# Optimization experiments

Measured on AMD Instinct MI355X. Metric: run time of the kernel, lower is better.

The kernel has to match this reference:

```python
import jax, jax.numpy as jnp
import numpy as np

DIM = 768
NUM_HEADS = 12
HEAD_DIM = DIM // NUM_HEADS
SCALE = HEAD_DIM ** -0.5
B, N = 8, 1024


def setup_inputs() -> dict:
    key = jax.random.key(0)
    k1, k2, k3, k4, k5 = jax.random.split(key, 5)
    x = jax.random.normal(k1, (B, N, DIM), dtype=jnp.float32)
    # qkv: Linear(dim, 3*dim, bias=False); proj: Linear(dim, dim) with bias
    w_qkv = jax.random.normal(k2, (3 * DIM, DIM), dtype=jnp.float32) * (DIM ** -0.5)
    w_proj = jax.random.normal(k3, (DIM, DIM), dtype=jnp.float32) * (DIM ** -0.5)
    b_proj = jnp.zeros((DIM,), dtype=jnp.float32)
    # learned attention mask parameter, shape (H, L, L) with L >= N
    att_mask = jax.random.normal(k4, (NUM_HEADS, N, N), dtype=jnp.float32)
    return {"x": x, "w_qkv": w_qkv, "w_proj": w_proj, "b_proj": b_proj, "att_mask": att_mask}


def reference(x, w_qkv, w_proj, b_proj, att_mask):
    Bx, Nx, C = x.shape
    # qkv projection -> (3, B, H, N, head_dim)
    qkv = (x @ w_qkv.T).reshape(Bx, Nx, 3, NUM_HEADS, C // NUM_HEADS)
    qkv = jnp.transpose(qkv, (2, 0, 3, 1, 4))
    q, k, v = qkv[0], qkv[1], qkv[2]  # gpd_ratio==active_ratio==1 -> scaling factor 1
    # scores [B, H, N, N]
    attn = jnp.einsum('bhnd,bhmd->bhnm', q, k) * SCALE
    # custom sigmoid mask gating before softmax (broadcast over batch)
    attn = attn * jax.nn.sigmoid(att_mask[:, :Nx, :Nx])[None, :, :, :]
    attn = jax.nn.softmax(attn, axis=-1)
    out = jnp.einsum('bhnm,bhmd->bhnd', attn, v)
    out = jnp.transpose(out, (0, 2, 1, 3)).reshape(Bx, Nx, C)
    return out @ w_proj.T + b_proj
```

## Files before the change

kernel.cpp:

```cpp
#include <hip/hip_runtime.h>
#include <math.h>
#include <stdint.h>

typedef unsigned short u16;
typedef __attribute__((ext_vector_type(8))) short short8;
typedef __attribute__((ext_vector_type(4))) float f32x4;

#define GATE_SCALE 0.18033688011112042f

#if __has_builtin(__builtin_amdgcn_exp2f)
#define FEXP2(x) __builtin_amdgcn_exp2f(x)
#else
#define FEXP2(x) exp2f(x)
#endif

__device__ __forceinline__ u16 f2b(float f) {
    union { float f; unsigned u; } v; v.f = f;
    unsigned r = v.u + 0x7fffu + ((v.u >> 16) & 1u);
    return (u16)(r >> 16);
}
__device__ __forceinline__ u16 f2b_hu(float f) {
    union { float f; unsigned u; } v; v.f = f;
    return (u16)((v.u + 0x8000u) >> 16);
}
__device__ __forceinline__ float b2f(u16 u) {
    union { float f; unsigned u; } v; v.u = ((unsigned)u) << 16; return v.f;
}

#define GLL16(gsrc, ldsbase) __builtin_amdgcn_global_load_lds(                    \
    (__attribute__((address_space(1))) void*)(uintptr_t)(gsrc),                   \
    (__attribute__((address_space(3))) void*)(uint32_t)(uintptr_t)(ldsbase),      \
    16, 0, 0)

#define NX4  1572864
#define NW14 442368
#define NW24 147456
#define NXW4 (NX4 + NW14 + NW24)

__global__ __launch_bounds__(256) void prep_xw(
    const float4* __restrict__ x, const float4* __restrict__ wq,
    const float4* __restrict__ wp,
    ushort4* __restrict__ xb, ushort4* __restrict__ wqb,
    ushort4* __restrict__ wpb)
{
    size_t i = (size_t)blockIdx.x * 256 + threadIdx.x;
    float4 v; ushort4* dst; size_t j;
    if (i < NX4)            { j = i;               v = x[j];  dst = xb;  }
    else if (i < NX4 + NW14){ j = i - NX4;         v = wq[j]; dst = wqb; }
    else                    { j = i - (NX4 + NW14);v = wp[j]; dst = wpb; }
    ushort4 o; o.x = f2b(v.x); o.y = f2b(v.y); o.z = f2b(v.z); o.w = f2b(v.w);
    dst[j] = o;
}

__global__ __launch_bounds__(256) void prep_gate(
    const float4* __restrict__ mask4, u16* __restrict__ gp)
{
    __shared__ u16 L[64][72];
    const int bid = blockIdx.x;
    const int kt = bid & 15, qt = (bid >> 4) & 15, h = bid >> 8;
    const int t = threadIdx.x;

    #pragma unroll
    for (int s = 0; s < 4; ++s) {
        const int idx = t + s * 256;
        const int row = idx >> 4, c4 = idx & 15;
        float4 v = mask4[(size_t)(h * 1024 + qt * 64 + row) * 256 + kt * 16 + c4];
        L[row][c4 * 4 + 0] = f2b(GATE_SCALE / (1.f + __expf(-v.x)));
        L[row][c4 * 4 + 1] = f2b(GATE_SCALE / (1.f + __expf(-v.y)));
        L[row][c4 * 4 + 2] = f2b(GATE_SCALE / (1.f + __expf(-v.z)));
        L[row][c4 * 4 + 3] = f2b(GATE_SCALE / (1.f + __expf(-v.w)));
    }
    __syncthreads();

    const int w = t >> 6, l = t & 63;
    const int fq = l >> 4, fr = l & 15;
    union { u16 u[16]; float4 f[2]; } vals;
    #pragma unroll
    for (int i = 0; i < 4; ++i)
        #pragma unroll
        for (int nt = 0; nt < 4; ++nt)
            vals.u[i * 4 + nt] = L[16 * w + 4 * fq + i][nt * 16 + fr];
    float4* dst = (float4*)(gp + (size_t)bid * 4096 + (size_t)t * 16);
    dst[0] = vals.f[0];
    dst[1] = vals.f[1];
}

__global__ __launch_bounds__(256) void qkv_gemm(
    const u16* __restrict__ xb, const u16* __restrict__ wb,
    u16* __restrict__ qb, u16* __restrict__ kb, u16* __restrict__ vb)
{
    __shared__ u16 As[3][4096];
    __shared__ u16 Bs[3][4096];
    const int t = threadIdx.x, l = t & 63, w = t >> 6;
    const int wm = (w & 1) * 64, wn = (w >> 1) * 64;

    const int orig = blockIdx.x + 18 * blockIdx.y;
    const int nid = (orig & 7) * 144 + (orig >> 3);
    const int m0 = (nid / 18) * 128, c0 = (nid % 18) * 128;

    f32x4 acc[4][4];
    #pragma unroll
    for (int i = 0; i < 4; ++i)
        #pragma unroll
        for (int j = 0; j < 4; ++j) { f32x4 z = {0.f,0.f,0.f,0.f}; acc[i][j] = z; }

    const int srow = l >> 2, sseg = l & 3;
    const int gcol = ((sseg ^ ((srow >> 1) & 3)) << 3);
    const u16* a0 = xb + (size_t)(m0 + w * 16 + srow) * 768 + gcol;
    const u16* a1 = a0 + (size_t)64 * 768;
    const u16* b0p = wb + (size_t)(c0 + w * 16 + srow) * 768 + gcol;
    const u16* b1p = b0p + (size_t)64 * 768;
    const int wofs = w * 512;

    const int fr = l & 15, fq = l >> 4;
    const int fseg = (fq ^ ((fr >> 1) & 3)) << 3;

    auto stage = [&](int bi, int koff) {
        GLL16(a0 + koff, &As[bi][wofs]);
        GLL16(a1 + koff, &As[bi][2048 + wofs]);
        GLL16(b0p + koff, &Bs[bi][wofs]);
        GLL16(b1p + koff, &Bs[bi][2048 + wofs]);
    };

    stage(0, 0);
    stage(1, 32);

    int cur = 0;
    for (int kt = 0; kt < 24; ++kt) {
        if (kt < 23) asm volatile("s_waitcnt vmcnt(4)" ::: "memory");
        else         asm volatile("s_waitcnt vmcnt(0)" ::: "memory");
        __builtin_amdgcn_s_barrier();
        if (kt < 22) {
            const int nn = (cur == 0) ? 2 : cur - 1;
            stage(nn, (kt + 2) * 32);
        }
        const u16* A = As[cur];
        const u16* B = Bs[cur];
        short8 af[4], bf[4];
        #pragma unroll
        for (int mt = 0; mt < 4; ++mt)
            af[mt] = *(const short8*)&A[(wm + mt * 16 + fr) * 32 + fseg];
        #pragma unroll
        for (int nt = 0; nt < 4; ++nt)
            bf[nt] = *(const short8*)&B[(wn + nt * 16 + fr) * 32 + fseg];
        #pragma unroll
        for (int mt = 0; mt < 4; ++mt)
            #pragma unroll
            for (int nt = 0; nt < 4; ++nt)
                acc[mt][nt] = __builtin_amdgcn_mfma_f32_16x16x32_bf16(
                    af[mt], bf[nt], acc[mt][nt], 0, 0, 0);
        cur = (cur == 2) ? 0 : cur + 1;
    }

    const int b = m0 >> 10;
    const int n0 = m0 & 1023;
    #pragma unroll
    for (int nt = 0; nt < 4; ++nt) {
        const int c = c0 + wn + nt * 16 + fr;
        const int which = c / 768;
        const int rem = c - which * 768;
        const int h = rem >> 6, d = rem & 63;
        if (which < 2) {
            u16* dst = ((which == 0) ? qb : kb)
                       + ((size_t)(b * 12 + h) * 1024) * 64 + d;
            #pragma unroll
            for (int mt = 0; mt < 4; ++mt)
                #pragma unroll
                for (int r = 0; r < 4; ++r) {
                    const int n = n0 + wm + mt * 16 + fq * 4 + r;
                    dst[(size_t)n * 64] = f2b(acc[mt][nt][r]);
                }
        } else {
            u16* dst = vb + ((size_t)(b * 12 + h) * 64 + d) * 1024
                          + n0 + wm + fq * 4;
            #pragma unroll
            for (int mt = 0; mt < 4; ++mt) {
                ushort4 pk;
                pk.x = f2b(acc[mt][nt][0]); pk.y = f2b(acc[mt][nt][1]);
                pk.z = f2b(acc[mt][nt][2]); pk.w = f2b(acc[mt][nt][3]);
                *(ushort4*)(dst + mt * 16) = pk;
            }
        }
    }
}

__global__ __launch_bounds__(256, 3) void flash_attn(
    const u16* __restrict__ qb, const u16* __restrict__ kb,
    const u16* __restrict__ vt, const u16* __restrict__ gperm,
    u16* __restrict__ aob)
{
    __shared__ u16 Qs[8192], Ks[4096], Vts[4096], Ps[4096];
    const int t = threadIdx.x, l = t & 63, w = t >> 6;
    const int bid = blockIdx.x;
    const int qtb = bid & 7, bh = bid >> 3;
    const int h = bh % 12, b = bh / 12;
    const int q0 = qtb * 128;

    const u16* hq = qb + (size_t)bh * 65536;
    const u16* hk = kb + (size_t)bh * 65536;
    const u16* hv = vt + (size_t)bh * 65536;
    const u16* hgb = gperm + ((size_t)h * 256 + qtb * 32) * 4096 + (w * 64 + l) * 16;

    const int sr = l >> 3, ss = l & 7;
    const int sg = ((ss ^ (sr & 7)) << 3);
    const int j0 = w * 2, j1 = j0 + 1;

    #pragma unroll
    for (int jq = 0; jq < 4; ++jq) {
        const int j = w * 4 + jq;
        GLL16(hq + (size_t)(q0 + j * 8 + sr) * 64 + sg, Qs + j * 512);
    }
    GLL16(hk + (size_t)(j0 * 8 + sr) * 64 + sg, Ks + j0 * 512);
    GLL16(hk + (size_t)(j1 * 8 + sr) * 64 + sg, Ks + j1 * 512);
    GLL16(hv + (size_t)(j0 * 8 + sr) * 1024 + sg, Vts + j0 * 512);
    GLL16(hv + (size_t)(j1 * 8 + sr) * 1024 + sg, Vts + j1 * 512);
    __syncthreads();

    const int fq = l >> 4, fr = l & 15;
    const int sega = ((fq ^ (fr & 7)) << 3);
    const int segb = (((4 + fq) ^ (fr & 7)) << 3);

    short8 aq[2][2];
    #pragma unroll
    for (int qh = 0; qh < 2; ++qh) {
        const int row = 16 * w + fr;
        aq[qh][0] = *(const short8*)&Qs[qh * 4096 + row * 64 + sega];
        aq[qh][1] = *(const short8*)&Qs[qh * 4096 + row * 64 + segb];
    }

    short8 gn[4];
    gn[0] = *(const short8*)(hgb);
    gn[1] = *(const short8*)(hgb + 8);
    gn[2] = *(const short8*)(hgb + 65536);
    gn[3] = *(const short8*)(hgb + 65536 + 8);

    float l_part[2][4] = {{0.f,0.f,0.f,0.f},{0.f,0.f,0.f,0.f}};
    f32x4 o[2][4];
    #pragma unroll
    for (int qh = 0; qh < 2; ++qh)
        #pragma unroll
        for (int nt = 0; nt < 4; ++nt) { f32x4 z = {0.f,0.f,0.f,0.f}; o[qh][nt] = z; }

    for (int kt = 0; kt < 16; ++kt) {
        short8 g[4];
        #pragma unroll
        for (int s = 0; s < 4; ++s) g[s] = gn[s];
        if (kt < 15) {
            const size_t go = (size_t)(kt + 1) * 4096;
            gn[0] = *(const short8*)(hgb + go);
            gn[1] = *(const short8*)(hgb + go + 8);
            gn[2] = *(const short8*)(hgb + 65536 + go);
            gn[3] = *(const short8*)(hgb + 65536 + go + 8);
        }

        f32x4 sv[2][4];
        #pragma unroll
        for (int nt = 0; nt < 4; ++nt) {
            short8 kf0 = *(const short8*)&Ks[(nt * 16 + fr) * 64 + sega];
            short8 kf1 = *(const short8*)&Ks[(nt * 16 + fr) * 64 + segb];
            f32x4 z0 = {0.f,0.f,0.f,0.f};
            z0 = __builtin_amdgcn_mfma_f32_16x16x32_bf16(aq[0][0], kf0, z0, 0, 0, 0);
            z0 = __builtin_amdgcn_mfma_f32_16x16x32_bf16(aq[0][1], kf1, z0, 0, 0, 0);
            sv[0][nt] = z0;
            f32x4 z1 = {0.f,0.f,0.f,0.f};
            z1 = __builtin_amdgcn_mfma_f32_16x16x32_bf16(aq[1][0], kf0, z1, 0, 0, 0);
            z1 = __builtin_amdgcn_mfma_f32_16x16x32_bf16(aq[1][1], kf1, z1, 0, 0, 0);
            sv[1][nt] = z1;
        }

        short8 ap[2][2];
        #pragma unroll
        for (int qh = 0; qh < 2; ++qh) {
            #pragma unroll
            for (int i = 0; i < 4; ++i) {
                const int pr = 4 * fq + i;
                #pragma unroll
                for (int nt = 0; nt < 4; ++nt) {
                    const int idx = i * 4 + nt;
                    const float gv = b2f((u16)(idx < 8 ? g[2 * qh][idx]
                                                       : g[2 * qh + 1][idx - 8]));
                    const float p = FEXP2(sv[qh][nt][i] * gv);
                    l_part[qh][i] += p;
                    const int col = nt * 16 + fr;
                    Ps[w * 1024 + pr * 64 + (((col >> 3) ^ (pr & 7)) << 3) + (col & 7)]
                        = f2b_hu(p);
                }
            }
            ap[qh][0] = *(const short8*)&Ps[w * 1024 + fr * 64 + sega];
            ap[qh][1] = *(const short8*)&Ps[w * 1024 + fr * 64 + segb];
        }

        #pragma unroll
        for (int nt = 0; nt < 4; ++nt) {
            short8 vf0 = *(const short8*)&Vts[(nt * 16 + fr) * 64 + sega];
            short8 vf1 = *(const short8*)&Vts[(nt * 16 + fr) * 64 + segb];
            o[0][nt] = __builtin_amdgcn_mfma_f32_16x16x32_bf16(ap[0][0], vf0, o[0][nt], 0, 0, 0);
            o[0][nt] = __builtin_amdgcn_mfma_f32_16x16x32_bf16(ap[0][1], vf1, o[0][nt], 0, 0, 0);
            o[1][nt] = __builtin_amdgcn_mfma_f32_16x16x32_bf16(ap[1][0], vf0, o[1][nt], 0, 0, 0);
            o[1][nt] = __builtin_amdgcn_mfma_f32_16x16x32_bf16(ap[1][1], vf1, o[1][nt], 0, 0, 0);
        }

        if (kt < 15) {
            __syncthreads();
            const size_t ko = (size_t)(kt + 1) * 64;
            GLL16(hk + (ko + j0 * 8 + sr) * 64 + sg, Ks + j0 * 512);
            GLL16(hk + (ko + j1 * 8 + sr) * 64 + sg, Ks + j1 * 512);
            GLL16(hv + (size_t)(j0 * 8 + sr) * 1024 + ko + sg, Vts + j0 * 512);
            GLL16(hv + (size_t)(j1 * 8 + sr) * 1024 + ko + sg, Vts + j1 * 512);
            __syncthreads();
        }
    }

    #pragma unroll
    for (int qh = 0; qh < 2; ++qh) {
        #pragma unroll
        for (int i = 0; i < 4; ++i) {
            float s = l_part[qh][i];
            s += __shfl_xor(s, 1, 16);
            s += __shfl_xor(s, 2, 16);
            s += __shfl_xor(s, 4, 16);
            s += __shfl_xor(s, 8, 16);
            const float inv = 1.f / s;
            const int n = q0 + qh * 64 + 16 * w + 4 * fq + i;
            const size_t rowoff = ((size_t)b * 1024 + n) * 768 + h * 64;
            #pragma unroll
            for (int nt = 0; nt < 4; ++nt)
                aob[rowoff + nt * 16 + fr] = f2b(o[qh][nt][i] * inv);
        }
    }
}

__global__ __launch_bounds__(256) void proj_gemm(
    const u16* __restrict__ aob, const u16* __restrict__ wb,
    const float* __restrict__ bproj, float* __restrict__ out)
{
    __shared__ u16 As[3][4096];
    __shared__ u16 Bs[3][4096];
    const int t = threadIdx.x, l = t & 63, w = t >> 6;
    const int wm = (w & 1) * 64, wn = (w >> 1) * 64;

    const int orig = blockIdx.x + 6 * blockIdx.y;
    const int nid = (orig & 7) * 48 + (orig >> 3);
    const int m0 = (nid / 6) * 128, c0 = (nid % 6) * 128;

    f32x4 acc[4][4];
    #pragma unroll
    for (int i = 0; i < 4; ++i)
        #pragma unroll
        for (int j = 0; j < 4; ++j) { f32x4 z = {0.f,0.f,0.f,0.f}; acc[i][j] = z; }

    const int srow = l >> 2, sseg = l & 3;
    const int gcol = ((sseg ^ ((srow >> 1) & 3)) << 3);
    const u16* a0 = aob + (size_t)(m0 + w * 16 + srow) * 768 + gcol;
    const u16* a1 = a0 + (size_t)64 * 768;
    const u16* b0p = wb + (size_t)(c0 + w * 16 + srow) * 768 + gcol;
    const u16* b1p = b0p + (size_t)64 * 768;
    const int wofs = w * 512;

    const int fr = l & 15, fq = l >> 4;
    const int fseg = (fq ^ ((fr >> 1) & 3)) << 3;

    auto stage = [&](int bi, int koff) {
        GLL16(a0 + koff, &As[bi][wofs]);
        GLL16(a1 + koff, &As[bi][2048 + wofs]);
        GLL16(b0p + koff, &Bs[bi][wofs]);
        GLL16(b1p + koff, &Bs[bi][2048 + wofs]);
    };

    stage(0, 0);
    stage(1, 32);

    int cur = 0;
    for (int kt = 0; kt < 24; ++kt) {
        if (kt < 23) asm volatile("s_waitcnt vmcnt(4)" ::: "memory");
        else         asm volatile("s_waitcnt vmcnt(0)" ::: "memory");
        __builtin_amdgcn_s_barrier();
        if (kt < 22) {
            const int nn = (cur == 0) ? 2 : cur - 1;
            stage(nn, (kt + 2) * 32);
        }
        const u16* A = As[cur];
        const u16* B = Bs[cur];
        short8 af[4], bf[4];
        #pragma unroll
        for (int mt = 0; mt < 4; ++mt)
            af[mt] = *(const short8*)&A[(wm + mt * 16 + fr) * 32 + fseg];
        #pragma unroll
        for (int nt = 0; nt < 4; ++nt)
            bf[nt] = *(const short8*)&B[(wn + nt * 16 + fr) * 32 + fseg];
        #pragma unroll
        for (int mt = 0; mt < 4; ++mt)
            #pragma unroll
            for (int nt = 0; nt < 4; ++nt)
                acc[mt][nt] = __builtin_amdgcn_mfma_f32_16x16x32_bf16(
                    af[mt], bf[nt], acc[mt][nt], 0, 0, 0);
        cur = (cur == 2) ? 0 : cur + 1;
    }

    #pragma unroll
    for (int nt = 0; nt < 4; ++nt) {
        const int c = c0 + wn + nt * 16 + fr;
        const float bias = bproj[c];
        #pragma unroll
        for (int mt = 0; mt < 4; ++mt)
            #pragma unroll
            for (int r = 0; r < 4; ++r) {
                const int m = m0 + wm + mt * 16 + fq * 4 + r;
                out[(size_t)m * 768 + c] = acc[mt][nt][r] + bias;
            }
    }
}

extern "C" void kernel_launch(void* const* d_in, const int* in_sizes, int n_in,
                              void* d_out, int out_size, void* d_ws, size_t ws_size,
                              hipStream_t stream)
{
    const float* x     = (const float*)d_in[0];
    const float* wqkv  = (const float*)d_in[1];
    const float* wproj = (const float*)d_in[2];
    const float* bproj = (const float*)d_in[3];
    const float* mask  = (const float*)d_in[4];
    float* out = (float*)d_out;

    char* ws = (char*)d_ws;
    u16* gperm  = (u16*)(ws);
    u16* xb     = (u16*)(ws + 25165824);
    u16* wqkvb  = (u16*)(ws + 37748736);
    u16* wprojb = (u16*)(ws + 41287680);
    u16* qb     = (u16*)(ws + 42467328);
    u16* kb     = (u16*)(ws + 55050240);
    u16* vb     = (u16*)(ws + 67633152);
    u16* aob    = (u16*)(ws + 80216064);

    prep_xw<<<NXW4 / 256, 256, 0, stream>>>(
        (const float4*)x, (const float4*)wqkv, (const float4*)wproj,
        (ushort4*)xb, (ushort4*)wqkvb, (ushort4*)wprojb);

    prep_gate<<<3072, 256, 0, stream>>>((const float4*)mask, gperm);

    qkv_gemm<<<dim3(18, 64), 256, 0, stream>>>(xb, wqkvb, qb, kb, vb);

    flash_attn<<<768, 256, 0, stream>>>(qb, kb, vb, gperm, aob);

    proj_gemm<<<dim3(6, 64), 256, 0, stream>>>(aob, wprojb, bproj, out);
}
```

Baseline: 242.5 us.

## Enlarge QKV GEMM tiles and read attention K/V/Q directly from global

The QKV GEMM moves from 128x128 tiles with 4 waves and triple buffering to 256x256 tiles with 8 waves and double buffering, waiting for all loads to finish each k-step. Flash attention drops its shared-memory staging of Q, K and V and loads the MFMA fragments straight from global memory, which removes the barriers and LDS traffic. The larger GEMM tile increases reuse, but the grid shrinks to 288 blocks and loads no longer overlap compute. The direct global reads in attention rely on L1/L2 for reuse across waves and can add memory latency that is not hidden.

```diff
diff --git a/kernel.cpp b/kernel.cpp
--- a/kernel.cpp
+++ b/kernel.cpp
@@ -85,78 +85,71 @@
     dst[1] = vals.f[1];
 }
 
-__global__ __launch_bounds__(256) void qkv_gemm(
+__global__ __launch_bounds__(512, 2) void qkv_gemm(
     const u16* __restrict__ xb, const u16* __restrict__ wb,
     u16* __restrict__ qb, u16* __restrict__ kb, u16* __restrict__ vb)
 {
-    __shared__ u16 As[3][4096];
-    __shared__ u16 Bs[3][4096];
+    __shared__ u16 As[2][8192];
+    __shared__ u16 Bs[2][8192];
     const int t = threadIdx.x, l = t & 63, w = t >> 6;
-    const int wm = (w & 1) * 64, wn = (w >> 1) * 64;
-
-    const int orig = blockIdx.x + 18 * blockIdx.y;
-    const int nid = (orig & 7) * 144 + (orig >> 3);
-    const int m0 = (nid / 18) * 128, c0 = (nid % 18) * 128;
-
-    f32x4 acc[4][4];
-    #pragma unroll
-    for (int i = 0; i < 4; ++i)
+    const int wr = (w >> 2) * 128, wc = (w & 3) * 64;
+
+    const int orig = blockIdx.x;
+    const int nid = (orig & 7) * 36 + (orig >> 3);
+    const int m0 = (nid / 9) * 256, c0 = (nid % 9) * 256;
+
+    f32x4 acc[8][4];
+    #pragma unroll
+    for (int i = 0; i < 8; ++i)
         #pragma unroll
         for (int j = 0; j < 4; ++j) { f32x4 z = {0.f,0.f,0.f,0.f}; acc[i][j] = z; }
 
     const int srow = l >> 2, sseg = l & 3;
     const int gcol = ((sseg ^ ((srow >> 1) & 3)) << 3);
-    const u16* a0 = xb + (size_t)(m0 + w * 16 + srow) * 768 + gcol;
-    const u16* a1 = a0 + (size_t)64 * 768;
-    const u16* b0p = wb + (size_t)(c0 + w * 16 + srow) * 768 + gcol;
-    const u16* b1p = b0p + (size_t)64 * 768;
+    const u16* aA0 = xb + (size_t)(m0 + w * 16 + srow) * 768 + gcol;
+    const u16* aA1 = aA0 + (size_t)128 * 768;
+    const u16* aB0 = wb + (size_t)(c0 + w * 16 + srow) * 768 + gcol;
+    const u16* aB1 = aB0 + (size_t)128 * 768;
     const int wofs = w * 512;
 
     const int fr = l & 15, fq = l >> 4;
     const int fseg = (fq ^ ((fr >> 1) & 3)) << 3;
 
     auto stage = [&](int bi, int koff) {
-        GLL16(a0 + koff, &As[bi][wofs]);
-        GLL16(a1 + koff, &As[bi][2048 + wofs]);
-        GLL16(b0p + koff, &Bs[bi][wofs]);
-        GLL16(b1p + koff, &Bs[bi][2048 + wofs]);
+        GLL16(aA0 + koff, &As[bi][wofs]);
+        GLL16(aA1 + koff, &As[bi][4096 + wofs]);
+        GLL16(aB0 + koff, &Bs[bi][wofs]);
+        GLL16(aB1 + koff, &Bs[bi][4096 + wofs]);
     };
 
     stage(0, 0);
-    stage(1, 32);
-
-    int cur = 0;
+
     for (int kt = 0; kt < 24; ++kt) {
-        if (kt < 23) asm volatile("s_waitcnt vmcnt(4)" ::: "memory");
-        else         asm volatile("s_waitcnt vmcnt(0)" ::: "memory");
+        asm volatile("s_waitcnt vmcnt(0)" ::: "memory");
         __builtin_amdgcn_s_barrier();
-        if (kt < 22) {
-            const int nn = (cur == 0) ? 2 : cur - 1;
-            stage(nn, (kt + 2) * 32);
-        }
-        const u16* A = As[cur];
-        const u16* B = Bs[cur];
-        short8 af[4], bf[4];
-        #pragma unroll
-        for (int mt = 0; mt < 4; ++mt)
-            af[mt] = *(const short8*)&A[(wm + mt * 16 + fr) * 32 + fseg];
+        if (kt < 23) stage((kt + 1) & 1, (kt + 1) * 32);
+        const u16* A = As[kt & 1];
+        const u16* B = Bs[kt & 1];
+        short8 af[8], bf[4];
+        #pragma unroll
+        for (int mt = 0; mt < 8; ++mt)
+            af[mt] = *(const short8*)&A[(wr + mt * 16 + fr) * 32 + fseg];
         #pragma unroll
         for (int nt = 0; nt < 4; ++nt)
-            bf[nt] = *(const short8*)&B[(wn + nt * 16 + fr) * 32 + fseg];
-        #pragma unroll
-        for (int mt = 0; mt < 4; ++mt)
+            bf[nt] = *(const short8*)&B[(wc + nt * 16 + fr) * 32 + fseg];
+        #pragma unroll
+        for (int mt = 0; mt < 8; ++mt)
             #pragma unroll
             for (int nt = 0; nt < 4; ++nt)
                 acc[mt][nt] = __builtin_amdgcn_mfma_f32_16x16x32_bf16(
                     af[mt], bf[nt], acc[mt][nt], 0, 0, 0);
-        cur = (cur == 2) ? 0 : cur + 1;
     }
 
     const int b = m0 >> 10;
     const int n0 = m0 & 1023;
     #pragma unroll
     for (int nt = 0; nt < 4; ++nt) {
-        const int c = c0 + wn + nt * 16 + fr;
+        const int c = c0 + wc + nt * 16 + fr;
         const int which = c / 768;
         const int rem = c - which * 768;
         const int h = rem >> 6, d = rem & 63;
@@ -164,17 +157,17 @@
             u16* dst = ((which == 0) ? qb : kb)
                        + ((size_t)(b * 12 + h) * 1024) * 64 + d;
             #pragma unroll
-            for (int mt = 0; mt < 4; ++mt)
+            for (int mt = 0; mt < 8; ++mt)
                 #pragma unroll
                 for (int r = 0; r < 4; ++r) {
-                    const int n = n0 + wm + mt * 16 + fq * 4 + r;
+                    const int n = n0 + wr + mt * 16 + fq * 4 + r;
                     dst[(size_t)n * 64] = f2b(acc[mt][nt][r]);
                 }
         } else {
             u16* dst = vb + ((size_t)(b * 12 + h) * 64 + d) * 1024
-                          + n0 + wm + fq * 4;
-            #pragma unroll
-            for (int mt = 0; mt < 4; ++mt) {
+                          + n0 + wr + fq * 4;
+            #pragma unroll
+            for (int mt = 0; mt < 8; ++mt) {
                 ushort4 pk;
                 pk.x = f2b(acc[mt][nt][0]); pk.y = f2b(acc[mt][nt][1]);
                 pk.z = f2b(acc[mt][nt][2]); pk.w = f2b(acc[mt][nt][3]);
@@ -189,7 +182,7 @@
     const u16* __restrict__ vt, const u16* __restrict__ gperm,
     u16* __restrict__ aob)
 {
-    __shared__ u16 Qs[8192], Ks[4096], Vts[4096], Ps[4096];
+    __shared__ u16 Ps[4096];
     const int t = threadIdx.x, l = t & 63, w = t >> 6;
     const int bid = blockIdx.x;
     const int qtb = bid & 7, bh = bid >> 3;
@@ -201,21 +194,6 @@
     const u16* hv = vt + (size_t)bh * 65536;
     const u16* hgb = gperm + ((size_t)h * 256 + qtb * 32) * 4096 + (w * 64 + l) * 16;
 
-    const int sr = l >> 3, ss = l & 7;
-    const int sg = ((ss ^ (sr & 7)) << 3);
-    const int j0 = w * 2, j1 = j0 + 1;
-
-    #pragma unroll
-    for (int jq = 0; jq < 4; ++jq) {
-        const int j = w * 4 + jq;
-        GLL16(hq + (size_t)(q0 + j * 8 + sr) * 64 + sg, Qs + j * 512);
-    }
-    GLL16(hk + (size_t)(j0 * 8 + sr) * 64 + sg, Ks + j0 * 512);
-    GLL16(hk + (size_t)(j1 * 8 + sr) * 64 + sg, Ks + j1 * 512);
-    GLL16(hv + (size_t)(j0 * 8 + sr) * 1024 + sg, Vts + j0 * 512);
-    GLL16(hv + (size_t)(j1 * 8 + sr) * 1024 + sg, Vts + j1 * 512);
-    __syncthreads();
-
     const int fq = l >> 4, fr = l & 15;
     const int sega = ((fq ^ (fr & 7)) << 3);
     const int segb = (((4 + fq) ^ (fr & 7)) << 3);
@@ -223,9 +201,9 @@
     short8 aq[2][2];
     #pragma unroll
     for (int qh = 0; qh < 2; ++qh) {
-        const int row = 16 * w + fr;
-        aq[qh][0] = *(const short8*)&Qs[qh * 4096 + row * 64 + sega];
-        aq[qh][1] = *(const short8*)&Qs[qh * 4096 + row * 64 + segb];
+        const u16* qrow = hq + (size_t)(q0 + qh * 64 + 16 * w + fr) * 64;
+        aq[qh][0] = *(const short8*)(qrow + fq * 8);
+        aq[qh][1] = *(const short8*)(qrow + 32 + fq * 8);
     }
 
     short8 gn[4];
@@ -256,8 +234,9 @@
         f32x4 sv[2][4];
         #pragma unroll
         for (int nt = 0; nt < 4; ++nt) {
-            short8 kf0 = *(const short8*)&Ks[(nt * 16 + fr) * 64 + sega];
-            short8 kf1 = *(const short8*)&Ks[(nt * 16 + fr) * 64 + segb];
+            const u16* krow = hk + (size_t)(kt * 64 + nt * 16 + fr) * 64;
+            short8 kf0 = *(const short8*)(krow + fq * 8);
+            short8 kf1 = *(const short8*)(krow + 32 + fq * 8);
             f32x4 z0 = {0.f,0.f,0.f,0.f};
             z0 = __builtin_amdgcn_mfma_f32_16x16x32_bf16(aq[0][0], kf0, z0, 0, 0, 0);
             z0 = __builtin_amdgcn_mfma_f32_16x16x32_bf16(aq[0][1], kf1, z0, 0, 0, 0);
@@ -292,22 +271,13 @@
 
         #pragma unroll
         for (int nt = 0; nt < 4; ++nt) {
-            short8 vf0 = *(const short8*)&Vts[(nt * 16 + fr) * 64 + sega];
-            short8 vf1 = *(const short8*)&Vts[(nt * 16 + fr) * 64 + segb];
+            const u16* vrow = hv + (size_t)(nt * 16 + fr) * 1024 + kt * 64;
+            short8 vf0 = *(const short8*)(vrow + fq * 8);
+            short8 vf1 = *(const short8*)(vrow + 32 + fq * 8);
             o[0][nt] = __builtin_amdgcn_mfma_f32_16x16x32_bf16(ap[0][0], vf0, o[0][nt], 0, 0, 0);
             o[0][nt] = __builtin_amdgcn_mfma_f32_16x16x32_bf16(ap[0][1], vf1, o[0][nt], 0, 0, 0);
             o[1][nt] = __builtin_amdgcn_mfma_f32_16x16x32_bf16(ap[1][0], vf0, o[1][nt], 0, 0, 0);
             o[1][nt] = __builtin_amdgcn_mfma_f32_16x16x32_bf16(ap[1][1], vf1, o[1][nt], 0, 0, 0);
-        }
-
-        if (kt < 15) {
-            __syncthreads();
-            const size_t ko = (size_t)(kt + 1) * 64;
-            GLL16(hk + (ko + j0 * 8 + sr) * 64 + sg, Ks + j0 * 512);
-            GLL16(hk + (ko + j1 * 8 + sr) * 64 + sg, Ks + j1 * 512);
-            GLL16(hv + (size_t)(j0 * 8 + sr) * 1024 + ko + sg, Vts + j0 * 512);
-            GLL16(hv + (size_t)(j1 * 8 + sr) * 1024 + ko + sg, Vts + j1 * 512);
-            __syncthreads();
         }
     }
 
@@ -438,7 +408,7 @@
 
     prep_gate<<<3072, 256, 0, stream>>>((const float4*)mask, gperm);
 
-    qkv_gemm<<<dim3(18, 64), 256, 0, stream>>>(xb, wqkvb, qb, kb, vb);
+    qkv_gemm<<<288, 512, 0, stream>>>(xb, wqkvb, qb, kb, vb);
 
     flash_attn<<<768, 256, 0, stream>>>(qb, kb, vb, gperm, aob);
 
```

Result: slower. 303.7 us (+25.3%).
